# Kernel optimization log

Measured on AMD Instinct MI355X. Metric: run time of the kernel, lower is better.

## Reference

```python
import jax, jax.numpy as jnp
import numpy as np

ALPHA = 1.0
BETA = 0.5
B, N, T = 4096, 32, 8
EPS = 1e-8


def _lsa_square(cost):
    """Jonker-Volgenant shortest augmenting path LSA on a square cost [n,n].
    Returns col_of_row[i] = column assigned to row i (same as scipy's
    linear_sum_assignment col_ind for square matrices)."""
    n = cost.shape[0]
    INF = np.inf
    u = np.zeros(n + 1)
    v = np.zeros(n + 1)
    p = np.zeros(n + 1, dtype=np.int64)   # p[j] = row matched to column j (1-based)
    way = np.zeros(n + 1, dtype=np.int64)
    for i in range(1, n + 1):
        p[0] = i
        j0 = 0
        minv = np.full(n + 1, INF)
        used = np.zeros(n + 1, dtype=bool)
        while True:
            used[j0] = True
            i0 = p[j0]
            # vectorized relaxation over all unused columns
            cur = cost[i0 - 1] - u[i0] - v[1:]
            free = ~used[1:]
            mv = minv[1:]
            wy = way[1:]
            upd = free & (cur < mv)
            mv[upd] = cur[upd]
            wy[upd] = j0
            masked = np.where(free, mv, INF)
            j1 = int(np.argmin(masked)) + 1
            delta = masked[j1 - 1]
            u[p[used]] += delta
            v[used] -= delta
            minv[~used] -= delta
            j0 = j1
            if p[j0] == 0:
                break
        while j0:
            j1 = way[j0]
            p[j0] = p[j1]
            j0 = j1
    col_of_row = np.empty(n, dtype=np.int32)
    for j in range(1, n + 1):
        col_of_row[p[j] - 1] = j - 1
    return col_of_row


def _batched_lsa(cost):
    cost = np.asarray(cost, dtype=np.float64)
    return np.stack([_lsa_square(c) for c in cost]).astype(np.int32)


def hungarian(cost):
    b, n = cost.shape[0], cost.shape[1]
    return jax.pure_callback(_batched_lsa, jax.ShapeDtypeStruct((b, n), jnp.int32), cost)


def _assignment(pred_j, logits, target_j, target_types):
    # j_cost[b,i,j] = |pred_j[b,i] - target_j[b,j]|
    j_cost = jnp.abs(pred_j[:, :, None] - target_j[:, None, :])
    # torch code uses -log(softmax + 1e-8) for the cost matrix (not log_softmax)
    logp = jnp.log(jax.nn.softmax(logits, axis=-1) + EPS)      # [B,N,T]
    idx = jnp.broadcast_to(target_types[:, None, :].astype(jnp.int32), j_cost.shape)
    type_cost = -jnp.take_along_axis(logp, idx, axis=-1)       # [B,N,N]
    cost = ALPHA * j_cost + BETA * type_cost
    return hungarian(jax.lax.stop_gradient(cost))              # [B,N] int32


def _matched_loss(pred_j, logits, target_j, target_types, cols):
    # row_ind == arange(N) for square full-mask case; cols = assigned targets
    tj = jnp.take_along_axis(target_j, cols.astype(jnp.int32), axis=1)        # [B,N]
    tt = jnp.take_along_axis(target_types, cols.astype(jnp.int64), axis=1)    # [B,N]
    j_loss = jnp.abs(pred_j - tj).sum()
    ls = jax.nn.log_softmax(logits, axis=-1)
    type_loss = -jnp.take_along_axis(ls, tt[..., None].astype(jnp.int32), axis=-1).sum()
    total = pred_j.shape[0] * pred_j.shape[1]
    loss = (ALPHA * j_loss + BETA * type_loss) / total
    j_mae = j_loss / total
    type_acc = (jnp.argmax(logits, axis=-1) == tt).astype(jnp.float32).mean()
    return loss, j_mae, type_acc


def setup_inputs() -> dict:
    key = jax.random.key(0)
    k1, k2, k3, k4 = jax.random.split(key, 4)
    return {
        'pred_j': jax.random.normal(k1, (B, N), dtype=jnp.float32),
        'pred_type_logits': jax.random.normal(k2, (B, N, T), dtype=jnp.float32),
        'target_j': jax.random.normal(k3, (B, N), dtype=jnp.float32),
        'target_types': jax.random.randint(k4, (B, N), 0, T, dtype=jnp.int64),
        'pred_mask': jnp.ones((B, N), dtype=bool),
        'target_mask': jnp.ones((B, N), dtype=bool),
    }


def reference(pred_j, pred_type_logits, target_j, target_types, pred_mask, target_mask):
    # Masks are all-ones here, so every slot is valid and the per-sample
    # torch loop vectorizes into one batched computation (same math).
    cols = _assignment(pred_j, pred_type_logits, target_j, target_types)
    loss, j_mae, type_acc = _matched_loss(pred_j, pred_type_logits, target_j, target_types, cols)
    return loss, j_mae, type_acc
```

## Files before the change

### kernel.cpp

```cpp
#include <hip/hip_runtime.h>
#include <math.h>


constexpr int BB = 4096;
constexpr int NN = 32;
constexpr int TT = 8;
constexpr float ALPHA_F = 1.0f;
constexpr float BETA_F  = 0.5f;
constexpr float EPS_F   = 1e-8f;

template <int CTRL, int ROW_MASK>
__device__ __forceinline__ float dpp_min(float x) {
    int t = __builtin_amdgcn_update_dpp(__float_as_int(x), __float_as_int(x),
                                        CTRL, ROW_MASK, 0xf, false);
    return fminf(x, __int_as_float(t));
}

__device__ __forceinline__ float wave32_min_bcast(float x) {
    x = dpp_min<0xB1,  0xf>(x);
    x = dpp_min<0x4E,  0xf>(x);
    x = dpp_min<0x124, 0xf>(x);
    x = dpp_min<0x128, 0xf>(x);
    x = dpp_min<0x142, 0xa>(x);
    return __int_as_float(__builtin_amdgcn_readlane(__float_as_int(x), 31));
}

__global__ __launch_bounds__(256) void hungarian_lsa_kernel(
    const float* __restrict__ pred_j,
    const float* __restrict__ logits,
    const float* __restrict__ target_j,
    const int*   __restrict__ target_types,
    double* __restrict__ partials)
{
    __shared__ float costS[4][NN * NN];
    __shared__ float cbcS [4][NN * NN];
    __shared__ float lgtS [4][NN * TT];

    const int wave = threadIdx.x >> 6;
    const int lane = threadIdx.x & 63;
    const int col  = lane & 31;
    const int b    = blockIdx.x * 4 + wave;

    float* cost = costS[wave];
    float* cbc  = cbcS[wave];
    float* lgp  = cbcS[wave];
    float* lgt  = lgtS[wave];

    const float pj = pred_j  [b * NN + col];
    const float tj = target_j[b * NN + col];
    const int   tt = target_types[b * NN + col];

    float x[TT];
    const float* lrow = logits + ((size_t)b * NN + col) * TT;
#pragma unroll
    for (int t = 0; t < TT; ++t) x[t] = lrow[t];

    float m = x[0]; int am = 0;
#pragma unroll
    for (int t = 1; t < TT; ++t) { if (x[t] > m) { m = x[t]; am = t; } }
    float s = 0.f;
#pragma unroll
    for (int t = 0; t < TT; ++t) s += expf(x[t] - m);
    const float lse = m + logf(s);

    if (lane < 32) {
#pragma unroll
        for (int t = 0; t < TT; ++t) {
            float p = expf(x[t] - m) / s;
            lgp[col * TT + t] = logf(p + EPS_F);
            lgt[col * TT + t] = x[t];
        }
    }
    __syncthreads();

    for (int i = 0; i < NN; ++i) {
        float pji = __shfl(pj, i);
        float lp  = lgp[i * TT + tt];
        float c   = ALPHA_F * fabsf(pji - tj) + BETA_F * (-lp);
        if (lane < 32) cost[i * NN + col] = c;
    }
    __syncthreads();

    const float INFF = __builtin_inff();
    float v_f  = 0.0f;
    float uc_f = 0.0f;
    int   p_i  = 0;
    unsigned amask = 0;

    float cr = cost[col];

    for (int i = 1; i <= NN; ++i) {
        bool used_b = false;

        float cur = cr - v_f;
        float mv  = wave32_min_bcast(cur);
        unsigned long long bm = __ballot(cur == mv);
        int   j1      = __ffsll(bm);
        float rowSum  = mv;

        while ((amask >> (j1 - 1)) & 1u) {
            const int j0 = j1;
            used_b |= (col == j0 - 1);
            const float uc_j0 = __shfl(uc_f, j0 - 1);
            const float cur2  = cbc[(j0 - 1) * NN + col] - v_f;
            const float curm  = used_b ? INFF : cur2;
            mv = wave32_min_bcast(curm);
            bm = __ballot((!used_b) && (cur2 == mv));
            j1 = __ffsll(bm);
            const float delta = mv - uc_j0;
            rowSum += delta;
            if (used_b) { v_f -= delta; uc_f += delta; }
        }

        if (col == j1 - 1) { p_i = i; uc_f = rowSum; }
        amask |= 1u << (j1 - 1);
        cbc[(j1 - 1) * NN + col] = cr;
        cr = cost[min(i, NN - 1) * NN + col];
    }

    const int   row      = p_i - 1;
    const float pj_row   = __shfl(pj,  row);
    const float lse_row  = __shfl(lse, row);
    const int   am_row   = __shfl(am,  row);
    const float logit_tt = lgt[row * TT + tt];

    double sj = (lane < 32) ? (double)fabsf(pj_row - tj)   : 0.0;
    double st = (lane < 32) ? (double)(lse_row - logit_tt) : 0.0;
    double sa = (lane < 32) ? ((am_row == tt) ? 1.0 : 0.0) : 0.0;
#pragma unroll
    for (int off = 32; off >= 1; off >>= 1) {
        sj += __shfl_xor(sj, off);
        st += __shfl_xor(st, off);
        sa += __shfl_xor(sa, off);
    }
    if (lane == 0) {
        partials[b * 3 + 0] = sj;
        partials[b * 3 + 1] = st;
        partials[b * 3 + 2] = sa;
    }
}

__global__ __launch_bounds__(256) void hungarian_finalize_kernel(
    const double* __restrict__ partials, float* __restrict__ out)
{
    __shared__ double sm0[256], sm1[256], sm2[256];
    const int tid = threadIdx.x;
    double a = 0.0, c = 0.0, e = 0.0;
    for (int i = tid; i < BB; i += 256) {
        a += partials[i * 3 + 0];
        c += partials[i * 3 + 1];
        e += partials[i * 3 + 2];
    }
    sm0[tid] = a; sm1[tid] = c; sm2[tid] = e;
    __syncthreads();
    for (int s = 128; s > 0; s >>= 1) {
        if (tid < s) {
            sm0[tid] += sm0[tid + s];
            sm1[tid] += sm1[tid + s];
            sm2[tid] += sm2[tid + s];
        }
        __syncthreads();
    }
    if (tid == 0) {
        const double jl = sm0[0], tl = sm1[0], ac = sm2[0];
        const double total = (double)BB * (double)NN;
        out[0] = (float)((jl + 0.5 * tl) / total);
        out[1] = (float)(jl / total);
        out[2] = (float)(ac / total);
    }
}

extern "C" void kernel_launch(void* const* d_in, const int* in_sizes, int n_in,
                              void* d_out, int out_size, void* d_ws, size_t ws_size,
                              hipStream_t stream) {
    const float* pred_j       = (const float*)d_in[0];
    const float* logits       = (const float*)d_in[1];
    const float* target_j     = (const float*)d_in[2];
    const int*   target_types = (const int*)  d_in[3];

    double* partials = (double*)d_ws;
    float*  out      = (float*)d_out;

    hungarian_lsa_kernel<<<BB / 4, 256, 0, stream>>>(
        pred_j, logits, target_j, target_types, partials);
    hungarian_finalize_kernel<<<1, 256, 0, stream>>>(partials, out);
}
```

Before: 49.53 us.

## Keep per-lane cost column in registers instead of LDS cost matrices

Each lane now keeps its cost column as a 32-entry register array, built with readlane broadcasts instead of shuffles. It drops the shared cost and assigned-row-cost matrices and a barrier. In the augmenting loop, the matched row of a column comes from a readlane of p_i, and its cost is selected from registers through a uniform-index switch. This removes LDS traffic and shrinks shared memory, in exchange for higher VGPR pressure and branchy selection code.

After: 62.11 us. 25.4% more time.

```diff
diff --git a/kernel.cpp b/kernel.cpp
--- a/kernel.cpp
+++ b/kernel.cpp
@@ -25,6 +25,17 @@
     return __int_as_float(__builtin_amdgcn_readlane(__float_as_int(x), 31));
 }
 
+__device__ __forceinline__ float readlane_f(float x, int lane) {
+    return __int_as_float(__builtin_amdgcn_readlane(__float_as_int(x), lane));
+}
+
+#define SEL4(B) case B+0: return cc[B+0]; case B+1: return cc[B+1]; \
+                case B+2: return cc[B+2]; case B+3: return cc[B+3];
+__device__ __forceinline__ float sel32(const float (&cc)[NN], int r) {
+    switch (r) { SEL4(0) SEL4(4) SEL4(8) SEL4(12) SEL4(16) SEL4(20) SEL4(24) SEL4(28) }
+    __builtin_unreachable();
+}
+
 __global__ __launch_bounds__(256) void hungarian_lsa_kernel(
     const float* __restrict__ pred_j,
     const float* __restrict__ logits,
@@ -32,19 +43,16 @@
     const int*   __restrict__ target_types,
     double* __restrict__ partials)
 {
-    __shared__ float costS[4][NN * NN];
-    __shared__ float cbcS [4][NN * NN];
-    __shared__ float lgtS [4][NN * TT];
+    __shared__ float lgpS[4][NN * TT];
+    __shared__ float lgtS[4][NN * TT];
 
     const int wave = threadIdx.x >> 6;
     const int lane = threadIdx.x & 63;
     const int col  = lane & 31;
     const int b    = blockIdx.x * 4 + wave;
 
-    float* cost = costS[wave];
-    float* cbc  = cbcS[wave];
-    float* lgp  = cbcS[wave];
-    float* lgt  = lgtS[wave];
+    float* lgp = lgpS[wave];
+    float* lgt = lgtS[wave];
 
     const float pj = pred_j  [b * NN + col];
     const float tj = target_j[b * NN + col];
@@ -73,13 +81,13 @@
     }
     __syncthreads();
 
-    for (int i = 0; i < NN; ++i) {
-        float pji = __shfl(pj, i);
-        float lp  = lgp[i * TT + tt];
-        float c   = ALPHA_F * fabsf(pji - tj) + BETA_F * (-lp);
-        if (lane < 32) cost[i * NN + col] = c;
+    float cc[NN];
+#pragma unroll
+    for (int r = 0; r < NN; ++r) {
+        const float pjr = readlane_f(pj, r);
+        const float lp  = lgp[r * TT + tt];
+        cc[r] = ALPHA_F * fabsf(pjr - tj) + BETA_F * (-lp);
     }
-    __syncthreads();
 
     const float INFF = __builtin_inff();
     float v_f  = 0.0f;
@@ -87,12 +95,10 @@
     int   p_i  = 0;
     unsigned amask = 0;
 
-    float cr = cost[col];
-
     for (int i = 1; i <= NN; ++i) {
         bool used_b = false;
 
-        float cur = cr - v_f;
+        float cur = sel32(cc, i - 1) - v_f;
         float mv  = wave32_min_bcast(cur);
         unsigned long long bm = __ballot(cur == mv);
         int   j1      = __ffsll(bm);
@@ -101,8 +107,9 @@
         while ((amask >> (j1 - 1)) & 1u) {
             const int j0 = j1;
             used_b |= (col == j0 - 1);
-            const float uc_j0 = __shfl(uc_f, j0 - 1);
-            const float cur2  = cbc[(j0 - 1) * NN + col] - v_f;
+            const int   r0    = __builtin_amdgcn_readlane(p_i, j0 - 1) - 1;
+            const float uc_j0 = readlane_f(uc_f, j0 - 1);
+            const float cur2  = sel32(cc, r0) - v_f;
             const float curm  = used_b ? INFF : cur2;
             mv = wave32_min_bcast(curm);
             bm = __ballot((!used_b) && (cur2 == mv));
@@ -114,8 +121,6 @@
 
         if (col == j1 - 1) { p_i = i; uc_f = rowSum; }
         amask |= 1u << (j1 - 1);
-        cbc[(j1 - 1) * NN + col] = cr;
-        cr = cost[min(i, NN - 1) * NN + col];
     }
 
     const int   row      = p_i - 1;
```
